# Performance work log

Hardware: AMD Instinct MI355X
Metric: run time of the kernel (lower is better)

## Reference

```python
import jax, jax.numpy as jnp
import numpy as np

B, NQ, NKV = 2, 1024, 4096
DQ = 1024          # query_dim == context_dim
H, DH = 16, 64     # heads, dim_head
INNER = H * DH     # 1024
SCALE = DH ** -0.5


def setup_inputs() -> dict:
    key = jax.random.key(0)
    ks = jax.random.split(key, 6)
    s = 1.0 / np.sqrt(DQ)
    return {
        "x": jax.random.normal(ks[0], (B, NQ, DQ), dtype=jnp.float32),
        "context": jax.random.normal(ks[1], (B, NKV, DQ), dtype=jnp.float32),
        "Wq": jax.random.normal(ks[2], (DQ, INNER), dtype=jnp.float32) * s,
        "Wkv": jax.random.normal(ks[3], (DQ, 2 * INNER), dtype=jnp.float32) * s,
        "Wout": jax.random.normal(ks[4], (INNER, DQ), dtype=jnp.float32) * (1.0 / np.sqrt(INNER)),
        "b_out": jax.random.normal(ks[5], (DQ,), dtype=jnp.float32) * 0.01,
    }


def _split_heads(t):
    # b n (h d) -> b h n d
    b, n, _ = t.shape
    return t.reshape(b, n, H, DH).transpose(0, 2, 1, 3)


def reference(x, context, Wq, Wkv, Wout, b_out):
    q = x @ Wq                       # [B, NQ, INNER]
    kv = context @ Wkv               # [B, NKV, 2*INNER]
    k, v = jnp.split(kv, 2, axis=-1)
    q, k, v = map(_split_heads, (q, k, v))          # [B, H, n, DH]
    sim = jnp.einsum("bhid,bhjd->bhij", q, k) * SCALE  # [B, H, NQ, NKV]
    attn = jax.nn.softmax(sim, axis=-1)
    out = jnp.einsum("bhij,bhjd->bhid", attn, v)       # [B, H, NQ, DH]
    out = out.transpose(0, 2, 1, 3).reshape(B, NQ, INNER)  # (b h) n d -> b n (h d)
    return out @ Wout + b_out
```

## Files before the change

### kernel.cpp

```cpp
#include <hip/hip_runtime.h>
#include <stdint.h>

#define B_    2
#define NQ_   1024
#define NKV_  4096
#define DQ_   1024
#define H_    16
#define DH_   64
#define INNER_ 1024

typedef unsigned short u16;
typedef uint32_t u32;
typedef __bf16 bf16x8 __attribute__((ext_vector_type(8)));
typedef float  f32x4  __attribute__((ext_vector_type(4)));

__device__ __forceinline__ u16 f2bf(float x) {
  union { float f; uint32_t u; } v; v.f = x;
  uint32_t r = v.u + 0x7FFFu + ((v.u >> 16) & 1u);
  return (u16)(r >> 16);
}
__device__ __forceinline__ u32 pack2(float a, float b) {
  return (u32)f2bf(a) | ((u32)f2bf(b) << 16);
}
__device__ __forceinline__ u32 pack2rn(float a, float b) {
  union { float f; u32 u; } x, y; x.f = a; y.f = b;
  return __builtin_amdgcn_perm(y.u + 0x8000u, x.u + 0x8000u, 0x07060302u);
}
__device__ __forceinline__ float bf2f(u16 s) {
  union { float f; uint32_t u; } v; v.u = ((uint32_t)s) << 16; return v.f;
}

__device__ __forceinline__ void gload16(const void* g, void* l) {
  __builtin_amdgcn_global_load_lds((const __attribute__((address_space(1))) void*)g,
                                   (__attribute__((address_space(3))) void*)l,
                                   16, 0, 0);
}

__global__ __launch_bounds__(256) void prep(const float* __restrict__ x,
                                            const float* __restrict__ ctx,
                                            const float* __restrict__ Wq,
                                            const float* __restrict__ Wkv,
                                            const float* __restrict__ Wout,
                                            u16* __restrict__ xb,
                                            u16* __restrict__ ctxb,
                                            u16* __restrict__ WqT,
                                            u16* __restrict__ WkvT,
                                            u16* __restrict__ WoutT) {
  int bid = blockIdx.x;
  if (bid < 10240) {
    const float* src; u16* dst; int blk;
    if (bid < 2048) { src = x; dst = xb; blk = bid; }
    else            { src = ctx; dst = ctxb; blk = bid - 2048; }
    int i = (blk * 256 + threadIdx.x) * 4;
    float4 v = *(const float4*)(src + i);
    uint2 o; o.x = pack2(v.x, v.y); o.y = pack2(v.z, v.w);
    *(uint2*)(dst + i) = o;
    return;
  }
  __shared__ float tile[32][33];
  const float* W; u16* Wt; int K, N, local, nsh;
  if (bid < 11264)      { W = Wq;   Wt = WqT;   K = 1024; N = 1024; local = bid - 10240; nsh = 5; }
  else if (bid < 13312) { W = Wkv;  Wt = WkvT;  K = 1024; N = 2048; local = bid - 11264; nsh = 6; }
  else                  { W = Wout; Wt = WoutT; K = 1024; N = 1024; local = bid - 13312; nsh = 5; }
  int n0 = (local & ((1 << nsh) - 1)) * 32;
  int k0 = (local >> nsh) * 32;
  int tx = threadIdx.x & 31, ty = threadIdx.x >> 5;
  for (int i = ty; i < 32; i += 8)
    tile[i][tx] = W[(size_t)(k0 + i) * N + n0 + tx];
  __syncthreads();
  for (int i = ty; i < 32; i += 8)
    Wt[(size_t)(n0 + i) * K + k0 + tx] = f2bf(tile[tx][i]);
}

__global__ __launch_bounds__(256) void qkv_gemm(const u16* __restrict__ xb,
                                                const u16* __restrict__ ctxb,
                                                const u16* __restrict__ WqT,
                                                const u16* __restrict__ WkvT,
                                                u16* __restrict__ qb,
                                                u16* __restrict__ kb,
                                                u16* __restrict__ vTb) {
  __shared__ __align__(16) u16 As[128 * 32];
  __shared__ __align__(16) u16 Bs[128 * 32];
  const int tid = threadIdx.x;
  const int lane = tid & 63;
  const int w = tid >> 6;
  const int wr = w >> 1, wc = w & 1;
  const int l15 = lane & 15, quad = lane >> 4;

  int bid = blockIdx.x;
  const u16 *A, *Bt; int m0, n0, mode;
  if (bid < 128) { m0 = (bid >> 3) * 128; n0 = (bid & 7) * 128; A = xb;   Bt = WqT;  mode = 0; }
  else { bid -= 128; m0 = (bid >> 4) * 128; n0 = (bid & 15) * 128; A = ctxb; Bt = WkvT;
         mode = (n0 < 1024) ? 1 : 2; }
  const int K = 1024;

  const u16* Ab = A + (size_t)m0 * K;
  const u16* Bb = Bt + (size_t)n0 * K;

  f32x4 acc[4][4] = {};

  const int q1 = w * 64 + lane;
  const int q2 = q1 + 256;
  const int ar1 = q1 >> 2, ac1 = (q1 & 3) << 3;
  const int ar2 = q2 >> 2, ac2 = (q2 & 3) << 3;

  for (int k0 = 0; k0 < K; k0 += 32) {
    __syncthreads();
    gload16(Ab + (size_t)ar1 * K + k0 + ac1, &As[w * 512]);
    gload16(Ab + (size_t)ar2 * K + k0 + ac2, &As[2048 + w * 512]);
    gload16(Bb + (size_t)ar1 * K + k0 + ac1, &Bs[w * 512]);
    gload16(Bb + (size_t)ar2 * K + k0 + ac2, &Bs[2048 + w * 512]);
    __syncthreads();
    bf16x8 af[4], bfr[4];
#pragma unroll
    for (int i = 0; i < 4; ++i)
      af[i] = *(const bf16x8*)&As[(wr * 64 + i * 16 + l15) * 32 + quad * 8];
#pragma unroll
    for (int j = 0; j < 4; ++j)
      bfr[j] = *(const bf16x8*)&Bs[(wc * 64 + j * 16 + l15) * 32 + quad * 8];
#pragma unroll
    for (int i = 0; i < 4; ++i)
#pragma unroll
      for (int j = 0; j < 4; ++j)
        acc[i][j] = __builtin_amdgcn_mfma_f32_16x16x32_bf16(af[i], bfr[j], acc[i][j], 0, 0, 0);
  }

  if (mode == 2) {
    const int bb = m0 >> 12;
#pragma unroll
    for (int i = 0; i < 4; ++i) {
      int kvr = (m0 & 4095) + wr * 64 + i * 16 + quad * 4;
#pragma unroll
      for (int j = 0; j < 4; ++j) {
        int c = (n0 - 1024) + wc * 64 + j * 16 + l15;
        int h = c >> 6, dh = c & 63;
        uint2 st;
        st.x = pack2(acc[i][j][0], acc[i][j][1]);
        st.y = pack2(acc[i][j][2], acc[i][j][3]);
        *(uint2*)&vTb[((size_t)((bb * 16 + h) * 64 + dh)) * NKV_ + kvr] = st;
      }
    }
    return;
  }

  u16* out = (mode == 0) ? qb : kb;
  const int N = 1024;
#pragma unroll
  for (int i = 0; i < 4; ++i)
#pragma unroll
    for (int j = 0; j < 4; ++j) {
      int col = n0 + wc * 64 + j * 16 + l15;
#pragma unroll
      for (int r = 0; r < 4; ++r) {
        int row = m0 + wr * 64 + i * 16 + quad * 4 + r;
        out[(size_t)row * N + col] = f2bf(acc[i][j][r]);
      }
    }
}

__global__ __launch_bounds__(256) void out_gemm(const u16* __restrict__ A,
                                                const u16* __restrict__ Bt,
                                                float* __restrict__ Cout,
                                                const float* __restrict__ bias) {
  __shared__ __align__(16) u16 As[64 * 32];
  __shared__ __align__(16) u16 Bs[128 * 32];
  const int tid = threadIdx.x;
  const int lane = tid & 63;
  const int w = tid >> 6;
  const int wr = w >> 1, wc = w & 1;
  const int l15 = lane & 15, quad = lane >> 4;
  const int unit = blockIdx.x;
  const int m0 = (unit >> 3) * 64, n0 = (unit & 7) * 128;
  const int K = 1024, N = 1024;

  const u16* Ab = A + (size_t)m0 * K;
  const u16* Bb = Bt + (size_t)n0 * K;
  f32x4 acc[2][4] = {};

  const int ar = tid >> 2, ac = (tid & 3) << 3;
  const int q1 = w * 64 + lane, q2 = q1 + 256;
  const int br1 = q1 >> 2, bc1 = (q1 & 3) << 3;
  const int br2 = q2 >> 2, bc2 = (q2 & 3) << 3;

  for (int k0 = 0; k0 < K; k0 += 32) {
    __syncthreads();
    gload16(Ab + (size_t)ar * K + k0 + ac, &As[w * 512]);
    gload16(Bb + (size_t)br1 * K + k0 + bc1, &Bs[w * 512]);
    gload16(Bb + (size_t)br2 * K + k0 + bc2, &Bs[2048 + w * 512]);
    __syncthreads();
    bf16x8 af[2], bfr[4];
#pragma unroll
    for (int i = 0; i < 2; ++i)
      af[i] = *(const bf16x8*)&As[(wr * 32 + i * 16 + l15) * 32 + quad * 8];
#pragma unroll
    for (int j = 0; j < 4; ++j)
      bfr[j] = *(const bf16x8*)&Bs[(wc * 64 + j * 16 + l15) * 32 + quad * 8];
#pragma unroll
    for (int i = 0; i < 2; ++i)
#pragma unroll
      for (int j = 0; j < 4; ++j)
        acc[i][j] = __builtin_amdgcn_mfma_f32_16x16x32_bf16(af[i], bfr[j], acc[i][j], 0, 0, 0);
  }

#pragma unroll
  for (int i = 0; i < 2; ++i)
#pragma unroll
    for (int j = 0; j < 4; ++j) {
      int col = n0 + wc * 64 + j * 16 + l15;
      float bv = bias[col];
#pragma unroll
      for (int r = 0; r < 4; ++r) {
        int row = m0 + wr * 32 + i * 16 + quad * 4 + r;
        Cout[(size_t)row * N + col] = acc[i][j][r] + bv;
      }
    }
}

__global__ __launch_bounds__(256, 2) void attn_kernel(const u16* __restrict__ qg,
                                                      const u16* __restrict__ kb,
                                                      const u16* __restrict__ vT,
                                                      u16* __restrict__ attn_out) {
  __shared__ __align__(16) u16 Ks[128 * 64];
  __shared__ __align__(16) u16 Vs[64 * 128];
  __shared__ __align__(16) u32 P32[4 * 4 * 16 * 20];
  __shared__ float Lr[4][4][16];

  const int tid = threadIdx.x;
  const int lane = tid & 63;
  const int w = tid >> 6;
  const int l15 = lane & 15, quad = lane >> 4;
  const int bh = blockIdx.x, b = bh >> 4, h = bh & 15;
  const int q0 = blockIdx.y * 64;

  const float SC = 0.125f * 1.44269504088896340736f;
  union { u16 s[8]; bf16x8 v; } qf[4][2];
#pragma unroll
  for (int t = 0; t < 4; ++t)
#pragma unroll
    for (int kc = 0; kc < 2; ++kc) {
      const u16* qp = qg + (size_t)(b * NQ_ + q0 + t * 16 + l15) * INNER_ + h * 64 +
                      kc * 32 + quad * 8;
      union { u16 s[8]; uint4 u; } tmp;
      tmp.u = *(const uint4*)qp;
#pragma unroll
      for (int e = 0; e < 8; ++e) qf[t][kc].s[e] = f2bf(bf2f(tmp.s[e]) * SC);
    }

  f32x4 Oacc[4][4] = {};
  float l_lane[4] = {0.f, 0.f, 0.f, 0.f};

  for (int it = 0; it < 32; ++it) {
    const int j0 = it * 128;
    __syncthreads();
#pragma unroll
    for (int i = 0; i < 4; ++i) {
      int s = i * 256 + tid;
      int kr = s >> 3, kg = (s ^ kr) & 7;
      gload16(kb + (size_t)(b * NKV_ + j0 + kr) * 1024 + h * 64 + kg * 8,
              &Ks[(i * 256 + w * 64) * 8]);
      int vr = s >> 4, vg = (s ^ vr) & 15;
      gload16(vT + (size_t)(bh * 64 + vr) * NKV_ + j0 + vg * 8,
              &Vs[(i * 256 + w * 64) * 8]);
    }
    __syncthreads();

    bf16x8 kf[2][2];
#pragma unroll
    for (int kvt = 0; kvt < 2; ++kvt)
#pragma unroll
      for (int kc = 0; kc < 2; ++kc)
        kf[kvt][kc] = *(const bf16x8*)
          &Ks[(w * 32 + kvt * 16 + l15) * 64 + (((kc * 4 + quad) ^ l15) & 7) * 8];
    f32x4 sacc[2][4] = {};
#pragma unroll
    for (int kvt = 0; kvt < 2; ++kvt)
#pragma unroll
      for (int t = 0; t < 4; ++t)
#pragma unroll
        for (int kc = 0; kc < 2; ++kc)
          sacc[kvt][t] = __builtin_amdgcn_mfma_f32_16x16x32_bf16(
              kf[kvt][kc], qf[t][kc].v, sacc[kvt][t], 0, 0, 0);

#pragma unroll
    for (int kvt = 0; kvt < 2; ++kvt)
#pragma unroll
      for (int t = 0; t < 4; ++t) {
        float p0 = __builtin_amdgcn_exp2f(sacc[kvt][t][0]);
        float p1 = __builtin_amdgcn_exp2f(sacc[kvt][t][1]);
        float p2 = __builtin_amdgcn_exp2f(sacc[kvt][t][2]);
        float p3 = __builtin_amdgcn_exp2f(sacc[kvt][t][3]);
        l_lane[t] += (p0 + p1) + (p2 + p3);
        uint2 pk; pk.x = pack2rn(p0, p1); pk.y = pack2rn(p2, p3);
        *(uint2*)&P32[((w * 4 + t) * 16 + l15) * 20 + kvt * 8 + quad * 2] = pk;
      }

    bf16x8 vf[4], pf[4];
#pragma unroll
    for (int d = 0; d < 4; ++d)
      vf[d] = *(const bf16x8*)
        &Vs[(d * 16 + l15) * 128 + (((w * 4 + quad) ^ l15) & 15) * 8];
#pragma unroll
    for (int t = 0; t < 4; ++t)
      pf[t] = *(const bf16x8*)&P32[((w * 4 + t) * 16 + l15) * 20 + quad * 4];
#pragma unroll
    for (int d = 0; d < 4; ++d)
#pragma unroll
      for (int t = 0; t < 4; ++t)
        Oacc[d][t] = __builtin_amdgcn_mfma_f32_16x16x32_bf16(vf[d], pf[t], Oacc[d][t],
                                                             0, 0, 0);
  }

#pragma unroll
  for (int t = 0; t < 4; ++t) {
    l_lane[t] += __shfl_xor(l_lane[t], 16);
    l_lane[t] += __shfl_xor(l_lane[t], 32);
  }
  if (quad == 0) {
#pragma unroll
    for (int t = 0; t < 4; ++t) Lr[w][t][l15] = l_lane[t];
  }
  __syncthreads();
  float inv = 1.0f / (Lr[0][w][l15] + Lr[1][w][l15] + Lr[2][w][l15] + Lr[3][w][l15]);

  float* red = (float*)P32;
  u16* ob = attn_out + (size_t)(b * NQ_ + q0 + w * 16 + l15) * INNER_ + h * 64;
#pragma unroll
  for (int d = 0; d < 4; ++d) {
    __syncthreads();
#pragma unroll
    for (int t = 0; t < 4; ++t)
      *(f32x4*)&red[(w * 4 + t) * 256 + quad * 64 + l15 * 4] = Oacc[d][t];
    __syncthreads();
    f32x4 r = *(const f32x4*)&red[(0 * 4 + w) * 256 + quad * 64 + l15 * 4];
#pragma unroll
    for (int ww = 1; ww < 4; ++ww) {
      f32x4 c = *(const f32x4*)&red[(ww * 4 + w) * 256 + quad * 64 + l15 * 4];
      r[0] += c[0]; r[1] += c[1]; r[2] += c[2]; r[3] += c[3];
    }
    *(u32*)(ob + d * 16 + quad * 4)     = pack2(r[0] * inv, r[1] * inv);
    *(u32*)(ob + d * 16 + quad * 4 + 2) = pack2(r[2] * inv, r[3] * inv);
  }
}

extern "C" void kernel_launch(void* const* d_in, const int* in_sizes, int n_in,
                              void* d_out, int out_size, void* d_ws, size_t ws_size,
                              hipStream_t stream) {
  const float* x    = (const float*)d_in[0];
  const float* ctx  = (const float*)d_in[1];
  const float* Wq   = (const float*)d_in[2];
  const float* Wkv  = (const float*)d_in[3];
  const float* Wout = (const float*)d_in[4];
  const float* bout = (const float*)d_in[5];

  char* ws = (char*)d_ws;
  u16* xb    = (u16*)(ws + (size_t)( 0u << 20));
  u16* ab    = (u16*)(ws + (size_t)( 0u << 20));
  u16* ctxb  = (u16*)(ws + (size_t)( 4u << 20));
  u16* WqT   = (u16*)(ws + (size_t)(20u << 20));
  u16* WkvT  = (u16*)(ws + (size_t)(22u << 20));
  u16* WoutT = (u16*)(ws + (size_t)(26u << 20));
  u16* qb    = (u16*)(ws + (size_t)(28u << 20));
  u16* kb    = (u16*)(ws + (size_t)(32u << 20));
  u16* vTb   = (u16*)(ws + (size_t)(48u << 20));

  prep<<<14336, 256, 0, stream>>>(x, ctx, Wq, Wkv, Wout, xb, ctxb, WqT, WkvT, WoutT);
  qkv_gemm<<<1152, 256, 0, stream>>>(xb, ctxb, WqT, WkvT, qb, kb, vTb);
  attn_kernel<<<dim3(32, 16), 256, 0, stream>>>(qb, kb, vTb, ab);
  out_gemm<<<256, 256, 0, stream>>>(ab, WoutT, (float*)d_out, bout);
}
```

Measured before the change: 227.2 us.

## Split QKV GEMM into pipelined 256x256 KV kernel and separate Q GEMM

Replaces the combined 128x128 QKV projection kernel with two kernels. The context-side KV projection uses 256x256 tiles, 512 threads, double-buffered LDS with XOR swizzling, a phased load/MFMA schedule with barriers, wave priority hints and an XCD-aware block remap. The query projection gets its own 64x128-tile kernel. The aim is to raise MFMA utilisation and data reuse on the largest GEMM. In exchange it adds an extra launch and uses large LDS (128KB per block), which limits occupancy.

```diff
diff --git a/kernel.cpp b/kernel.cpp
--- a/kernel.cpp
+++ b/kernel.cpp
@@ -72,88 +72,207 @@
     Wt[(size_t)(n0 + i) * K + k0 + tx] = f2bf(tile[tx][i]);
 }
 
-__global__ __launch_bounds__(256) void qkv_gemm(const u16* __restrict__ xb,
-                                                const u16* __restrict__ ctxb,
-                                                const u16* __restrict__ WqT,
-                                                const u16* __restrict__ WkvT,
-                                                u16* __restrict__ qb,
-                                                u16* __restrict__ kb,
-                                                u16* __restrict__ vTb) {
-  __shared__ __align__(16) u16 As[128 * 32];
+__global__ __launch_bounds__(512, 2) void kv_gemm(const u16* __restrict__ ctxb,
+                                                  const u16* __restrict__ WkvT,
+                                                  u16* __restrict__ kb,
+                                                  u16* __restrict__ vTb) {
+  __shared__ __align__(16) u16 As[2][256 * 64];
+  __shared__ __align__(16) u16 Bs[2][256 * 64];
+  const int tid = threadIdx.x;
+  const int lane = tid & 63;
+  const int w = tid >> 6;
+  const int wr = w >> 2, wc = w & 3;
+  const int l15 = lane & 15, quad = lane >> 4;
+  const int K = 1024;
+
+  int bid = blockIdx.x;
+  int wgid = (bid & 7) * 32 + (bid >> 3);
+  const int tm = wgid >> 3, tn = wgid & 7;
+  const int m0 = tm * 256, n0 = tn * 256;
+  const u16* Ag = ctxb + (size_t)m0 * K;
+  const u16* Bg = WkvT + (size_t)n0 * K;
+
+  size_t offA[2][2], offB[2][2];
+#pragma unroll
+  for (int ah = 0; ah < 2; ++ah)
+#pragma unroll
+    for (int p = 0; p < 2; ++p) {
+      int c = p * 512 + (w << 6) + lane;
+      int s = ah * 128 + (c >> 3);
+      int col = ((c & 7) ^ (s & 7)) << 3;
+      int rA = ((s >> 6) & 1) * 128 + ((s >> 7) & 1) * 64 + (s & 63);
+      int rB = ((s >> 5) & 3) * 64 + ((s >> 7) & 1) * 32 + (s & 31);
+      offA[ah][p] = (size_t)rA * 1024 + col;
+      offB[ah][p] = (size_t)rB * 1024 + col;
+    }
+
+#define STAGE_A(bufi, ah, kk) do { \
+    gload16(Ag + offA[ah][0] + (kk), &As[bufi][(ah) * 8192 + (w << 9)]); \
+    gload16(Ag + offA[ah][1] + (kk), &As[bufi][(ah) * 8192 + 4096 + (w << 9)]); \
+  } while (0)
+#define STAGE_B(bufi, bh, kk) do { \
+    gload16(Bg + offB[bh][0] + (kk), &Bs[bufi][(bh) * 8192 + (w << 9)]); \
+    gload16(Bg + offB[bh][1] + (kk), &Bs[bufi][(bh) * 8192 + 4096 + (w << 9)]); \
+  } while (0)
+#define LDA2(dst, i8, bufi) do { \
+    const int _s = ((i8) >> 2) * 128 + wr * 64 + ((i8) & 3) * 16 + l15; \
+    const u16* _p = &As[bufi][_s * 64]; const int _x = _s & 7; \
+    dst[0] = *(const bf16x8*)&_p[(quad ^ _x) << 3]; \
+    dst[1] = *(const bf16x8*)&_p[((quad + 4) ^ _x) << 3]; \
+  } while (0)
+#define LDB2(dst, j, bufi) do { \
+    const int _s = ((j) >> 1) * 128 + wc * 32 + ((j) & 1) * 16 + l15; \
+    const u16* _p = &Bs[bufi][_s * 64]; const int _x = _s & 7; \
+    dst[0] = *(const bf16x8*)&_p[(quad ^ _x) << 3]; \
+    dst[1] = *(const bf16x8*)&_p[((quad + 4) ^ _x) << 3]; \
+  } while (0)
+#define MF(i0, j0, bb) do { \
+    _Pragma("unroll") \
+    for (int _i = 0; _i < 4; ++_i) { \
+      acc[(i0) + _i][(j0)    ] = __builtin_amdgcn_mfma_f32_16x16x32_bf16(a[_i][0], bb[0][0], acc[(i0) + _i][(j0)    ], 0, 0, 0); \
+      acc[(i0) + _i][(j0)    ] = __builtin_amdgcn_mfma_f32_16x16x32_bf16(a[_i][1], bb[0][1], acc[(i0) + _i][(j0)    ], 0, 0, 0); \
+      acc[(i0) + _i][(j0) + 1] = __builtin_amdgcn_mfma_f32_16x16x32_bf16(a[_i][0], bb[1][0], acc[(i0) + _i][(j0) + 1], 0, 0, 0); \
+      acc[(i0) + _i][(j0) + 1] = __builtin_amdgcn_mfma_f32_16x16x32_bf16(a[_i][1], bb[1][1], acc[(i0) + _i][(j0) + 1], 0, 0, 0); \
+    } \
+  } while (0)
+
+  f32x4 acc[8][4] = {};
+  bf16x8 a[4][2], b[2][2], c2[2][2];
+
+  STAGE_A(0, 0, 0);
+  STAGE_B(0, 0, 0);
+  STAGE_B(0, 1, 0);
+  STAGE_A(0, 1, 0);
+  asm volatile("s_waitcnt vmcnt(4)" ::: "memory");
+  __builtin_amdgcn_s_barrier();
+
+#define KTILE(cur, nxt, kk, STG, W1, W2) do { \
+     \
+    LDB2(b[0], 0, cur); LDB2(b[1], 1, cur); \
+    LDA2(a[0], 0, cur); LDA2(a[1], 1, cur); LDA2(a[2], 2, cur); LDA2(a[3], 3, cur); \
+    if (STG) STAGE_A(nxt, 0, kk); \
+    __builtin_amdgcn_s_barrier(); \
+    asm volatile("s_waitcnt lgkmcnt(0)" ::: "memory"); \
+    __builtin_amdgcn_s_setprio(1); MF(0, 0, b); __builtin_amdgcn_s_setprio(0); \
+    asm volatile("s_waitcnt " W1 ::: "memory"); \
+    __builtin_amdgcn_s_barrier(); \
+     \
+    LDB2(c2[0], 2, cur); LDB2(c2[1], 3, cur); \
+    if (STG) STAGE_B(nxt, 0, kk); \
+    __builtin_amdgcn_s_barrier(); \
+    asm volatile("s_waitcnt lgkmcnt(0)" ::: "memory"); \
+    __builtin_amdgcn_s_setprio(1); MF(0, 2, c2); __builtin_amdgcn_s_setprio(0); \
+    asm volatile("s_waitcnt " W2 ::: "memory"); \
+    __builtin_amdgcn_s_barrier(); \
+     \
+    LDA2(a[0], 4, cur); LDA2(a[1], 5, cur); LDA2(a[2], 6, cur); LDA2(a[3], 7, cur); \
+    if (STG) STAGE_B(nxt, 1, kk); \
+    __builtin_amdgcn_s_barrier(); \
+    asm volatile("s_waitcnt lgkmcnt(0)" ::: "memory"); \
+    __builtin_amdgcn_s_setprio(1); MF(4, 0, b); __builtin_amdgcn_s_setprio(0); \
+    __builtin_amdgcn_s_barrier(); \
+     \
+    if (STG) STAGE_A(nxt, 1, kk); \
+    __builtin_amdgcn_s_barrier(); \
+    __builtin_amdgcn_s_setprio(1); MF(4, 2, c2); __builtin_amdgcn_s_setprio(0); \
+    if (STG) { asm volatile("s_waitcnt vmcnt(4)" ::: "memory"); } \
+    __builtin_amdgcn_s_barrier(); \
+  } while (0)
+
+  for (int T = 0; T < 15; ++T) {
+    const int cur = T & 1, nxt = cur ^ 1, kk = (T + 1) * 64;
+    KTILE(cur, nxt, kk, 1, "vmcnt(4)", "vmcnt(4)");
+  }
+  KTILE(1, 0, 0, 0, "vmcnt(2)", "vmcnt(0)");
+
+  if (tn < 4) {
+#pragma unroll
+    for (int i8 = 0; i8 < 8; ++i8)
+#pragma unroll
+      for (int j = 0; j < 4; ++j) {
+        int col = n0 + wc * 64 + j * 16 + l15;
+#pragma unroll
+        for (int r = 0; r < 4; ++r) {
+          int row = m0 + wr * 128 + i8 * 16 + quad * 4 + r;
+          kb[(size_t)row * 1024 + col] = f2bf(acc[i8][j][r]);
+        }
+      }
+  } else {
+    const int bb_ = m0 >> 12;
+#pragma unroll
+    for (int i8 = 0; i8 < 8; ++i8) {
+      int kvr = (m0 & 4095) + wr * 128 + i8 * 16 + quad * 4;
+#pragma unroll
+      for (int j = 0; j < 4; ++j) {
+        int c = (n0 - 1024) + wc * 64 + j * 16 + l15;
+        int h = c >> 6, dh = c & 63;
+        uint2 st;
+        st.x = pack2(acc[i8][j][0], acc[i8][j][1]);
+        st.y = pack2(acc[i8][j][2], acc[i8][j][3]);
+        *(uint2*)&vTb[((size_t)((bb_ * 16 + h) * 64 + dh)) * NKV_ + kvr] = st;
+      }
+    }
+  }
+#undef STAGE_A
+#undef STAGE_B
+#undef LDA2
+#undef LDB2
+#undef MF
+#undef KTILE
+}
+
+__global__ __launch_bounds__(256) void q_gemm(const u16* __restrict__ A,
+                                              const u16* __restrict__ Bt,
+                                              u16* __restrict__ outp) {
+  __shared__ __align__(16) u16 As[64 * 32];
   __shared__ __align__(16) u16 Bs[128 * 32];
   const int tid = threadIdx.x;
   const int lane = tid & 63;
   const int w = tid >> 6;
   const int wr = w >> 1, wc = w & 1;
   const int l15 = lane & 15, quad = lane >> 4;
-
-  int bid = blockIdx.x;
-  const u16 *A, *Bt; int m0, n0, mode;
-  if (bid < 128) { m0 = (bid >> 3) * 128; n0 = (bid & 7) * 128; A = xb;   Bt = WqT;  mode = 0; }
-  else { bid -= 128; m0 = (bid >> 4) * 128; n0 = (bid & 15) * 128; A = ctxb; Bt = WkvT;
-         mode = (n0 < 1024) ? 1 : 2; }
-  const int K = 1024;
+  const int unit = blockIdx.x;
+  const int m0 = (unit >> 3) * 64, n0 = (unit & 7) * 128;
+  const int K = 1024, N = 1024;
 
   const u16* Ab = A + (size_t)m0 * K;
   const u16* Bb = Bt + (size_t)n0 * K;
-
-  f32x4 acc[4][4] = {};
-
-  const int q1 = w * 64 + lane;
-  const int q2 = q1 + 256;
-  const int ar1 = q1 >> 2, ac1 = (q1 & 3) << 3;
-  const int ar2 = q2 >> 2, ac2 = (q2 & 3) << 3;
+  f32x4 acc[2][4] = {};
+
+  const int ar = tid >> 2, ac = (tid & 3) << 3;
+  const int q1 = w * 64 + lane, q2 = q1 + 256;
+  const int br1 = q1 >> 2, bc1 = (q1 & 3) << 3;
+  const int br2 = q2 >> 2, bc2 = (q2 & 3) << 3;
 
   for (int k0 = 0; k0 < K; k0 += 32) {
     __syncthreads();
-    gload16(Ab + (size_t)ar1 * K + k0 + ac1, &As[w * 512]);
-    gload16(Ab + (size_t)ar2 * K + k0 + ac2, &As[2048 + w * 512]);
-    gload16(Bb + (size_t)ar1 * K + k0 + ac1, &Bs[w * 512]);
-    gload16(Bb + (size_t)ar2 * K + k0 + ac2, &Bs[2048 + w * 512]);
-    __syncthreads();
-    bf16x8 af[4], bfr[4];
-#pragma unroll
-    for (int i = 0; i < 4; ++i)
-      af[i] = *(const bf16x8*)&As[(wr * 64 + i * 16 + l15) * 32 + quad * 8];
+    gload16(Ab + (size_t)ar * K + k0 + ac, &As[w * 512]);
+    gload16(Bb + (size_t)br1 * K + k0 + bc1, &Bs[w * 512]);
+    gload16(Bb + (size_t)br2 * K + k0 + bc2, &Bs[2048 + w * 512]);
+    __syncthreads();
+    bf16x8 af[2], bfr[4];
+#pragma unroll
+    for (int i = 0; i < 2; ++i)
+      af[i] = *(const bf16x8*)&As[(wr * 32 + i * 16 + l15) * 32 + quad * 8];
 #pragma unroll
     for (int j = 0; j < 4; ++j)
       bfr[j] = *(const bf16x8*)&Bs[(wc * 64 + j * 16 + l15) * 32 + quad * 8];
 #pragma unroll
-    for (int i = 0; i < 4; ++i)
+    for (int i = 0; i < 2; ++i)
 #pragma unroll
       for (int j = 0; j < 4; ++j)
         acc[i][j] = __builtin_amdgcn_mfma_f32_16x16x32_bf16(af[i], bfr[j], acc[i][j], 0, 0, 0);
   }
 
-  if (mode == 2) {
-    const int bb = m0 >> 12;
-#pragma unroll
-    for (int i = 0; i < 4; ++i) {
-      int kvr = (m0 & 4095) + wr * 64 + i * 16 + quad * 4;
-#pragma unroll
-      for (int j = 0; j < 4; ++j) {
-        int c = (n0 - 1024) + wc * 64 + j * 16 + l15;
-        int h = c >> 6, dh = c & 63;
-        uint2 st;
-        st.x = pack2(acc[i][j][0], acc[i][j][1]);
-        st.y = pack2(acc[i][j][2], acc[i][j][3]);
-        *(uint2*)&vTb[((size_t)((bb * 16 + h) * 64 + dh)) * NKV_ + kvr] = st;
-      }
-    }
-    return;
-  }
-
-  u16* out = (mode == 0) ? qb : kb;
-  const int N = 1024;
-#pragma unroll
-  for (int i = 0; i < 4; ++i)
+#pragma unroll
+  for (int i = 0; i < 2; ++i)
 #pragma unroll
     for (int j = 0; j < 4; ++j) {
       int col = n0 + wc * 64 + j * 16 + l15;
 #pragma unroll
       for (int r = 0; r < 4; ++r) {
-        int row = m0 + wr * 64 + i * 16 + quad * 4 + r;
-        out[(size_t)row * N + col] = f2bf(acc[i][j][r]);
+        int row = m0 + wr * 32 + i * 16 + quad * 4 + r;
+        outp[(size_t)row * N + col] = f2bf(acc[i][j][r]);
       }
     }
 }
@@ -364,7 +483,8 @@
   u16* vTb   = (u16*)(ws + (size_t)(48u << 20));
 
   prep<<<14336, 256, 0, stream>>>(x, ctx, Wq, Wkv, Wout, xb, ctxb, WqT, WkvT, WoutT);
-  qkv_gemm<<<1152, 256, 0, stream>>>(xb, ctxb, WqT, WkvT, qb, kb, vTb);
+  q_gemm<<<256, 256, 0, stream>>>(xb, WqT, qb);
+  kv_gemm<<<256, 512, 0, stream>>>(ctxb, WkvT, kb, vTb);
   attn_kernel<<<dim3(32, 16), 256, 0, stream>>>(qb, kb, vTb, ab);
   out_gemm<<<256, 256, 0, stream>>>(ab, WoutT, (float*)d_out, bout);
 }
```

Measured after the change: 228.3 us. Within noise of the previous version (+0.5%).
